# Optimization experiments

Hardware: AMD Instinct MI355X
Metric: run time of the kernel (lower is better)

The kernel has to match this reference:

```python
import jax, jax.numpy as jnp
import numpy as np

B, H, W, K = 48, 512, 512, 33
NEG_WEIGHT = 1.0


def _hann2d(k):
    n = np.arange(k)
    hw = 0.5 * (1.0 - np.cos(2.0 * np.pi * n / (k - 1)))  # torch.hann_window(periodic=False)
    return (hw[:, None] * hw[None, :]).astype(np.float32)


def setup_inputs() -> dict:
    key = jax.random.key(0)
    pred = jax.random.normal(key, (B, H, W), dtype=jnp.float32)
    rng = np.random.default_rng(0)
    ys = rng.integers(0, H - K, size=B)
    xs = rng.integers(0, W - K, size=B)
    tgt = np.zeros((B, H, W), dtype=np.float32)
    for i in range(B):
        tgt[i, ys[i]:ys[i] + K, xs[i]:xs[i] + K] = 1.0
    return {
        "pred": pred,
        "target": jnp.asarray(tgt),
        "hann_kernel": jnp.asarray(_hann2d(K)),
    }


def reference(pred, target, hann_kernel):
    h, w = pred.shape[1], pred.shape[2]

    def per_image_weights(t):
        m = (t == 1.0)
        ymin = jnp.argmax(jnp.any(m, axis=1))  # first row containing a 1
        xmin = jnp.argmax(jnp.any(m, axis=0))  # first col containing a 1
        wts = jnp.zeros((h, w), dtype=pred.dtype)
        wts = jax.lax.dynamic_update_slice(wts, hann_kernel, (ymin, xmin))
        wts = wts / wts.sum()
        is_zero = (wts == 0)
        neg_w = NEG_WEIGHT / is_zero.sum()
        wts = jnp.where(is_zero, neg_w, wts)
        return wts / wts.sum()

    weights = jax.vmap(per_image_weights)(target)  # [B,H,W]
    # BCEWithLogits (stable): logaddexp(0, x) - x*t
    bce = jnp.logaddexp(0.0, pred) - pred * target
    return jnp.mean(jnp.sum(bce * weights, axis=(1, 2)))
```

## Files before the change

### kernel.cpp

```cpp
#include <hip/hip_runtime.h>

#define NB 48
#define NH 512
#define NW 512
#define NK 33
#define HWSZ (NH * NW)
#define SLICES 32
#define ROWS_PER_BLK (NH / SLICES)
#define NBLK (NB * SLICES)


__device__ __forceinline__ float softplus(float x) {
  return fmaxf(x, 0.f) + __logf(1.f + __expf(-fabsf(x)));
}

__global__ void __launch_bounds__(256) stream_kernel(
    const float* __restrict__ pred, const float* __restrict__ tgt,
    int* __restrict__ wsi, float* __restrict__ partial) {
  const int tid = threadIdx.x;
  const int bid = blockIdx.x;
  const int b = bid >> 5;
  const int slice = bid & 31;

  if (bid < NB) {
    __shared__ int s_yh, s_xh, s_ymin, s_xmin;
    if (tid == 0) { s_ymin = NH; s_xmin = NW; }
    __syncthreads();
    const float* t = tgt + (size_t)bid * HWSZ;
    const int y = (tid >> 4) * NK;
    const int x = (tid & 15) * NK;
    if (t[y * NW + x] == 1.0f) { s_yh = y; s_xh = x; }
    __syncthreads();
    const int yh = s_yh, xh = s_xh;
    if (tid < NK) {
      const int yy = yh - (NK - 1) + tid;
      if (yy >= 0 && t[yy * NW + xh] == 1.0f) atomicMin(&s_ymin, yy);
    } else if (tid >= 64 && tid < 64 + NK) {
      const int xx = xh - (NK - 1) + (tid - 64);
      if (xx >= 0 && t[yh * NW + xx] == 1.0f) atomicMin(&s_xmin, xx);
    }
    __syncthreads();
    if (tid == 0) {
      wsi[2 * bid + 0] = s_ymin;
      wsi[2 * bid + 1] = s_xmin;
    }
  }

  const float4* p4 = reinterpret_cast<const float4*>(
      pred + (size_t)b * HWSZ + (slice * ROWS_PER_BLK) * NW);
  float acc = 0.f;
#pragma unroll
  for (int it = 0; it < 8; ++it) {
    const float4 pv = p4[it * 256 + tid];
    acc += softplus(pv.x) + softplus(pv.y) + softplus(pv.z) + softplus(pv.w);
  }
#pragma unroll
  for (int off = 32; off; off >>= 1) acc += __shfl_down(acc, off);
  __shared__ float s_red[4];
  if ((tid & 63) == 0) s_red[tid >> 6] = acc;
  __syncthreads();
  if (tid == 0)
    partial[128 + bid] = s_red[0] + s_red[1] + s_red[2] + s_red[3];
}

__global__ void __launch_bounds__(256) finish_kernel(
    const float* __restrict__ pred, const float* __restrict__ hann,
    const int* __restrict__ wsi, const float* __restrict__ partial,
    float* __restrict__ out) {
  const int b = blockIdx.x;
  const int tid = threadIdx.x;

  const int ymin = wsi[2 * b + 0];
  const int xmin = wsi[2 * b + 1];
  const float* pimg = pred + (size_t)b * HWSZ;

  float hsum = 0.f, hnnz = 0.f;
  for (int i = tid; i < NK * NK; i += 256) {
    const float h = hann[i];
    hsum += h;
    hnnz += (h != 0.f) ? 1.f : 0.f;
  }
  float psum = (tid < SLICES) ? partial[128 + SLICES * b + tid] : 0.f;
#pragma unroll
  for (int off = 32; off; off >>= 1) {
    hsum += __shfl_down(hsum, off);
    hnnz += __shfl_down(hnnz, off);
    psum += __shfl_down(psum, off);
  }
  __shared__ float s_red[12];
  if ((tid & 63) == 0) {
    s_red[tid >> 6] = hsum;
    s_red[4 + (tid >> 6)] = hnnz;
    s_red[8 + (tid >> 6)] = psum;
  }
  __syncthreads();
  const float S = s_red[0] + s_red[1] + s_red[2] + s_red[3];
  const float nnz = s_red[4] + s_red[5] + s_red[6] + s_red[7];
  const float psum_all = s_red[8];
  const float wpos_s = 1.0f / (2.0f * S * (float)NB);
  const float negw = 1.0f / (2.0f * ((float)HWSZ - nnz) * (float)NB);

  float corr = 0.f;
  for (int idx = tid; idx < NK * NK; idx += 256) {
    const int r = idx / NK;
    const int cx = idx - r * NK;
    const float px = pimg[(ymin + r) * NW + xmin + cx];
    const float hv = hann[idx];
    const float w = (hv != 0.f) ? hv * wpos_s : negw;
    corr += (w - negw) * softplus(px) - w * px;
  }
#pragma unroll
  for (int off = 32; off; off >>= 1) corr += __shfl_down(corr, off);
  if ((tid & 63) == 0) s_red[tid >> 6] = corr;
  __syncthreads();
  if (tid == 0) {
    const float image_loss =
        negw * psum_all + s_red[0] + s_red[1] + s_red[2] + s_red[3];
    atomicAdd(out, image_loss);
  }
}

extern "C" void kernel_launch(void* const* d_in, const int* in_sizes, int n_in,
                              void* d_out, int out_size, void* d_ws, size_t ws_size,
                              hipStream_t stream) {
  const float* pred = (const float*)d_in[0];
  const float* tgt  = (const float*)d_in[1];
  const float* hann = (const float*)d_in[2];
  int* wsi = (int*)d_ws;
  float* wsf = (float*)d_ws;
  stream_kernel<<<NBLK, 256, 0, stream>>>(pred, tgt, wsi, wsf);
  finish_kernel<<<NB, 256, 0, stream>>>(pred, hann, wsi, wsf, (float*)d_out);
}
```

Measured before the change: 117.1 us.

## Fuse stream and finish kernels into one launch with direct atomic accumulation

Merges the two kernels into a single launch. The first NB blocks locate the box, compute the hann statistics and add the window correction term. The remaining blocks stream softplus over pred, compute the negative weight locally via a ballot count of nonzero hann entries, and atomically add their scaled partial sums directly to the output. This removes the second kernel launch, the workspace round-trip and the dependency between the two stages. In exchange it adds about 1500 float atomics to a single address and redundant hann scanning in every streaming block.

Measured after the change: 127.5 us. 1.09x slower.

```diff
diff --git a/kernel.cpp b/kernel.cpp
--- a/kernel.cpp
+++ b/kernel.cpp
@@ -7,29 +7,35 @@
 #define HWSZ (NH * NW)
 #define SLICES 32
 #define ROWS_PER_BLK (NH / SLICES)
-#define NBLK (NB * SLICES)
-
+#define NSTREAM (NB * SLICES)
+#define NTOT (NSTREAM + NB)
 
 __device__ __forceinline__ float softplus(float x) {
   return fmaxf(x, 0.f) + __logf(1.f + __expf(-fabsf(x)));
 }
 
-__global__ void __launch_bounds__(256) stream_kernel(
+__global__ void __launch_bounds__(256) hanning_loss_kernel(
     const float* __restrict__ pred, const float* __restrict__ tgt,
-    int* __restrict__ wsi, float* __restrict__ partial) {
+    const float* __restrict__ hann, float* __restrict__ out) {
   const int tid = threadIdx.x;
   const int bid = blockIdx.x;
-  const int b = bid >> 5;
-  const int slice = bid & 31;
 
   if (bid < NB) {
+    const int b = bid;
     __shared__ int s_yh, s_xh, s_ymin, s_xmin;
+    __shared__ float s_red[12];
     if (tid == 0) { s_ymin = NH; s_xmin = NW; }
     __syncthreads();
-    const float* t = tgt + (size_t)bid * HWSZ;
+    const float* t = tgt + (size_t)b * HWSZ;
     const int y = (tid >> 4) * NK;
     const int x = (tid & 15) * NK;
     if (t[y * NW + x] == 1.0f) { s_yh = y; s_xh = x; }
+    float hsum = 0.f, hnnz = 0.f;
+    for (int i = tid; i < NK * NK; i += 256) {
+      const float h = hann[i];
+      hsum += h;
+      hnnz += (h != 0.f) ? 1.f : 0.f;
+    }
     __syncthreads();
     const int yh = s_yh, xh = s_xh;
     if (tid < NK) {
@@ -39,84 +45,66 @@
       const int xx = xh - (NK - 1) + (tid - 64);
       if (xx >= 0 && t[yh * NW + xx] == 1.0f) atomicMin(&s_xmin, xx);
     }
+#pragma unroll
+    for (int off = 32; off; off >>= 1) {
+      hsum += __shfl_down(hsum, off);
+      hnnz += __shfl_down(hnnz, off);
+    }
+    if ((tid & 63) == 0) { s_red[tid >> 6] = hsum; s_red[4 + (tid >> 6)] = hnnz; }
     __syncthreads();
-    if (tid == 0) {
-      wsi[2 * bid + 0] = s_ymin;
-      wsi[2 * bid + 1] = s_xmin;
+    const int ymin = s_ymin, xmin = s_xmin;
+    const float S = s_red[0] + s_red[1] + s_red[2] + s_red[3];
+    const float nnz = s_red[4] + s_red[5] + s_red[6] + s_red[7];
+    const float wpos_s = 1.0f / (2.0f * S * (float)NB);
+    const float negw = 1.0f / (2.0f * ((float)HWSZ - nnz) * (float)NB);
+    const float* pimg = pred + (size_t)b * HWSZ;
+    float corr = 0.f;
+    for (int idx = tid; idx < NK * NK; idx += 256) {
+      const int r = idx / NK;
+      const int cx = idx - r * NK;
+      const float px = pimg[(ymin + r) * NW + xmin + cx];
+      const float hv = hann[idx];
+      const float w = (hv != 0.f) ? hv * wpos_s : negw;
+      corr += (w - negw) * softplus(px) - w * px;
     }
-  }
-
-  const float4* p4 = reinterpret_cast<const float4*>(
-      pred + (size_t)b * HWSZ + (slice * ROWS_PER_BLK) * NW);
-  float acc = 0.f;
 #pragma unroll
-  for (int it = 0; it < 8; ++it) {
-    const float4 pv = p4[it * 256 + tid];
-    acc += softplus(pv.x) + softplus(pv.y) + softplus(pv.z) + softplus(pv.w);
-  }
+    for (int off = 32; off; off >>= 1) corr += __shfl_down(corr, off);
+    if ((tid & 63) == 0) s_red[8 + (tid >> 6)] = corr;
+    __syncthreads();
+    if (tid == 0)
+      atomicAdd(out, s_red[8] + s_red[9] + s_red[10] + s_red[11]);
+  } else {
+    const int sbid = bid - NB;
+    const int b = sbid >> 5;
+    const int slice = sbid & 31;
+    const float4* p4 = reinterpret_cast<const float4*>(
+        pred + (size_t)b * HWSZ + (slice * ROWS_PER_BLK) * NW);
+    float acc = 0.f;
 #pragma unroll
-  for (int off = 32; off; off >>= 1) acc += __shfl_down(acc, off);
-  __shared__ float s_red[4];
-  if ((tid & 63) == 0) s_red[tid >> 6] = acc;
-  __syncthreads();
-  if (tid == 0)
-    partial[128 + bid] = s_red[0] + s_red[1] + s_red[2] + s_red[3];
-}
-
-__global__ void __launch_bounds__(256) finish_kernel(
-    const float* __restrict__ pred, const float* __restrict__ hann,
-    const int* __restrict__ wsi, const float* __restrict__ partial,
-    float* __restrict__ out) {
-  const int b = blockIdx.x;
-  const int tid = threadIdx.x;
-
-  const int ymin = wsi[2 * b + 0];
-  const int xmin = wsi[2 * b + 1];
-  const float* pimg = pred + (size_t)b * HWSZ;
-
-  float hsum = 0.f, hnnz = 0.f;
-  for (int i = tid; i < NK * NK; i += 256) {
-    const float h = hann[i];
-    hsum += h;
-    hnnz += (h != 0.f) ? 1.f : 0.f;
-  }
-  float psum = (tid < SLICES) ? partial[128 + SLICES * b + tid] : 0.f;
+    for (int it = 0; it < 8; ++it) {
+      const float4 pv = p4[it * 256 + tid];
+      acc += softplus(pv.x) + softplus(pv.y) + softplus(pv.z) + softplus(pv.w);
+    }
+    const int lane = tid & 63;
+    const int wid = tid >> 6;
+    float negw = 0.f;
+    if (wid == 0) {
+      unsigned nnzc = 0;
 #pragma unroll
-  for (int off = 32; off; off >>= 1) {
-    hsum += __shfl_down(hsum, off);
-    hnnz += __shfl_down(hnnz, off);
-    psum += __shfl_down(psum, off);
-  }
-  __shared__ float s_red[12];
-  if ((tid & 63) == 0) {
-    s_red[tid >> 6] = hsum;
-    s_red[4 + (tid >> 6)] = hnnz;
-    s_red[8 + (tid >> 6)] = psum;
-  }
-  __syncthreads();
-  const float S = s_red[0] + s_red[1] + s_red[2] + s_red[3];
-  const float nnz = s_red[4] + s_red[5] + s_red[6] + s_red[7];
-  const float psum_all = s_red[8];
-  const float wpos_s = 1.0f / (2.0f * S * (float)NB);
-  const float negw = 1.0f / (2.0f * ((float)HWSZ - nnz) * (float)NB);
-
-  float corr = 0.f;
-  for (int idx = tid; idx < NK * NK; idx += 256) {
-    const int r = idx / NK;
-    const int cx = idx - r * NK;
-    const float px = pimg[(ymin + r) * NW + xmin + cx];
-    const float hv = hann[idx];
-    const float w = (hv != 0.f) ? hv * wpos_s : negw;
-    corr += (w - negw) * softplus(px) - w * px;
-  }
+      for (int j = 0; j < 17; ++j) {
+        const int idx = lane + 64 * j;
+        const bool nz = (idx < NK * NK) && (hann[idx] != 0.f);
+        nnzc += (unsigned)__popcll(__ballot(nz));
+      }
+      negw = 1.0f / (2.0f * ((float)HWSZ - (float)nnzc) * (float)NB);
+    }
 #pragma unroll
-  for (int off = 32; off; off >>= 1) corr += __shfl_down(corr, off);
-  if ((tid & 63) == 0) s_red[tid >> 6] = corr;
-  __syncthreads();
-  if (tid == 0) {
-    const float image_loss =
-        negw * psum_all + s_red[0] + s_red[1] + s_red[2] + s_red[3];
-    atomicAdd(out, image_loss);
+    for (int off = 32; off; off >>= 1) acc += __shfl_down(acc, off);
+    __shared__ float s_red[4];
+    if (lane == 0) s_red[wid] = acc;
+    __syncthreads();
+    if (tid == 0)
+      atomicAdd(out, negw * (s_red[0] + s_red[1] + s_red[2] + s_red[3]));
   }
 }
 
@@ -126,8 +114,5 @@
   const float* pred = (const float*)d_in[0];
   const float* tgt  = (const float*)d_in[1];
   const float* hann = (const float*)d_in[2];
-  int* wsi = (int*)d_ws;
-  float* wsf = (float*)d_ws;
-  stream_kernel<<<NBLK, 256, 0, stream>>>(pred, tgt, wsi, wsf);
-  finish_kernel<<<NB, 256, 0, stream>>>(pred, hann, wsi, wsf, (float*)d_out);
+  hanning_loss_kernel<<<NTOT, 256, 0, stream>>>(pred, tgt, hann, (float*)d_out);
 }
```
